# Optimization experiments

Hardware: AMD Instinct MI355X
Metric: run time of the kernel (lower is better)

Reference implementation:

```python
import jax, jax.numpy as jnp
import numpy as np

B, N, S = 32, 1000, 200
D, H, DK, FF, NL = 128, 8, 16, 512, 3
HK = H * DK


def _mha(x, Wq, Wk, Wv, Wo, bo):
    # x: [B, L, D]; manual multi-head attention matching the torch code
    Bv, L, _ = x.shape
    q = (x @ Wq).reshape(Bv, L, H, DK).transpose(0, 2, 1, 3)  # [B,H,L,dk]
    k = (x @ Wk).reshape(Bv, L, H, DK).transpose(0, 2, 1, 3)
    v = (x @ Wv).reshape(Bv, L, H, DK).transpose(0, 2, 1, 3)
    score = jnp.einsum('bhid,bhjd->bhij', q, k) / jnp.sqrt(jnp.asarray(DK, x.dtype))
    w = jax.nn.softmax(score, axis=-1)
    o = jnp.einsum('bhij,bhjd->bhid', w, v).transpose(0, 2, 1, 3).reshape(Bv, L, HK)
    return o @ Wo + bo


def _decoder_layer(x, Wq, Wk, Wv, Wo, bo, W1, b1, W2, b2):
    out1 = x + _mha(x, Wq, Wk, Wv, Wo, bo)
    ff = jax.nn.relu(out1 @ W1 + b1) @ W2 + b2
    return out1 + ff


def _forward(data, attention_bias, Wfirst, bfirst, Wlast, blast,
             Wq, Wk, Wv, Wo, bo, W1, b1, W2, b2, Wfin, bfin, sel):
    Bv, Np, Dm = data.shape
    Sn = sel.shape[1]
    bidx = jnp.arange(Bv)
    # _get_new_data: ordered list of unselected node indices, shape [B, N-S]
    mask = jnp.zeros((Bv, Np), bool).at[bidx[:, None], sel].set(True)
    vals = jnp.where(mask, Np, jnp.arange(Np)[None, :])
    unselect = jnp.sort(vals, axis=1)[:, : Np - Sn]            # [B, N-S]
    left = jnp.take_along_axis(data, unselect[:, :, None], axis=1)  # [B, N-S, D]
    # _get_encoding for first / last selected node
    first = data[bidx, sel[:, 0]]
    last = data[bidx, sel[:, -1]]
    ef = first @ Wfirst + bfirst
    el = last @ Wlast + blast
    out = jnp.concatenate([ef[:, None], left, el[:, None]], axis=1)  # [B, N-S+2, D]
    for i in range(Wq.shape[0]):
        out = _decoder_layer(out, Wq[i], Wk[i], Wv[i], Wo[i], bo[i],
                             W1[i], b1[i], W2[i], b2[i])
    logits = (out @ Wfin + bfin)[..., 0]                       # [B, N-S+2]
    # attention bias of current (last selected) node, gathered at unselected
    ab_cur = attention_bias[bidx, sel[:, -1]]                  # [B, N]
    ab_uns = jnp.take_along_axis(ab_cur, unselect, axis=1)     # [B, N-S]
    logits = logits.at[:, 1:-1].add(ab_uns)
    L = logits.shape[1]
    pos = jnp.arange(L)
    end_mask = (pos == 0) | (pos == L - 1)
    logits = jnp.where(end_mask[None, :], -jnp.inf, logits)
    props = jax.nn.softmax(logits, axis=-1)[:, 1:-1]           # [B, N-S]
    props = jnp.where(props <= 1e-5, props + 1e-7, props)
    # scatter back: selected positions -> -2, unselected -> props
    new_props = jnp.full((Bv, Np), -2.0, dtype=data.dtype)
    new_props = new_props.at[bidx[:, None], unselect].set(props)
    return new_props


def setup_inputs() -> dict:
    key = jax.random.key(0)
    ks = jax.random.split(key, 24)
    data = jax.random.normal(ks[0], (B, N, D), jnp.float32)
    # selected_node_list must contain unique indices per row (partial tour)
    sel = jax.vmap(lambda k: jax.random.permutation(k, N))(
        jax.random.split(ks[1], B))[:, :S].astype(jnp.int32)
    attention_bias = jax.random.normal(ks[2], (B, N, N), jnp.float32)

    def lin(k, shape, fan_in):
        return jax.random.normal(k, shape, jnp.float32) / np.float32(np.sqrt(fan_in))

    return dict(
        data=data,
        attention_bias=attention_bias,
        Wfirst=lin(ks[3], (D, D), D), bfirst=jnp.zeros((D,), jnp.float32),
        Wlast=lin(ks[4], (D, D), D), blast=jnp.zeros((D,), jnp.float32),
        Wq=lin(ks[5], (NL, D, HK), D),
        Wk=lin(ks[6], (NL, D, HK), D),
        Wv=lin(ks[7], (NL, D, HK), D),
        Wo=lin(ks[8], (NL, HK, D), HK), bo=jnp.zeros((NL, D), jnp.float32),
        W1=lin(ks[9], (NL, D, FF), D), b1=jnp.zeros((NL, FF), jnp.float32),
        W2=lin(ks[10], (NL, FF, D), FF), b2=jnp.zeros((NL, D), jnp.float32),
        Wfin=lin(ks[11], (D, 1), D), bfin=jnp.zeros((1,), jnp.float32),
        selected_node_list=sel,
    )


def reference(data, attention_bias, Wfirst, bfirst, Wlast, blast,
              Wq, Wk, Wv, Wo, bo, W1, b1, W2, b2, Wfin, bfin,
              selected_node_list):
    return _forward(data, attention_bias, Wfirst, bfirst, Wlast, blast,
                    Wq, Wk, Wv, Wo, bo, W1, b1, W2, b2, Wfin, bfin,
                    selected_node_list)
```

## Files before the change

### kernel.cpp

```cpp
#include <hip/hip_runtime.h>
#include <hip/hip_bf16.h>
#include <math.h>

#define NB 32
#define NN 1000
#define SS 200
#define DD 128
#define HH 8
#define DKK 16
#define FFD 512
#define NLAYER 3
#define LQ 802
#define LPAD 832
#define MROWS (NB*LQ)
#define NBLK64 (MROWS/64)
#define NQT 26
#define HSTR 516

typedef __attribute__((ext_vector_type(8))) short short8;
typedef __attribute__((ext_vector_type(4))) short short4v;
typedef __attribute__((ext_vector_type(16))) float f32x16;

static __device__ __forceinline__ unsigned short f2bf(float x) {
  union { float f; unsigned int u; } v; v.f = x;
  unsigned int r = v.u + 0x7fff + ((v.u >> 16) & 1);
  return (unsigned short)(r >> 16);
}

#define WCH 196608
__global__ __launch_bounds__(256) void k_wconv(const float* __restrict__ Wq, const float* __restrict__ Wk,
                       const float* __restrict__ Wv, const float* __restrict__ Wo,
                       const float* __restrict__ W1, const float* __restrict__ W2,
                       unsigned short* __restrict__ WtQKV, unsigned short* __restrict__ Wot,
                       unsigned short* __restrict__ W1t, unsigned short* __restrict__ W2t) {
  int e = blockIdx.x*256 + threadIdx.x;
  if (e >= 3*WCH) return;
  int layer = e / WCH, r = e - layer*WCH;
  if (r < 49152) {
    int n = r >> 7, k = r & 127;
    int sect = n >> 7, nn = n & 127;
    const float* W = (sect == 0) ? Wq : (sect == 1) ? Wk : Wv;
    WtQKV[layer*49152 + r] = f2bf(W[layer*16384 + k*128 + nn]);
  } else if (r < 65536) {
    int r2 = r - 49152;
    int n = r2 >> 7, k = r2 & 127;
    Wot[layer*16384 + r2] = f2bf(Wo[layer*16384 + k*128 + n]);
  } else if (r < 131072) {
    int r2 = r - 65536;
    int n = r2 >> 7, k = r2 & 127;
    W1t[layer*65536 + r2] = f2bf(W1[layer*65536 + k*512 + n]);
  } else {
    int r2 = r - 131072;
    int n = r2 >> 9, k = r2 & 511;
    W2t[layer*65536 + r2] = f2bf(W2[layer*65536 + k*128 + n]);
  }
}

__global__ __launch_bounds__(1024) void k_unselect(const int* __restrict__ sel,
                                                   int* __restrict__ unselect,
                                                   int* __restrict__ pos) {
  int b = blockIdx.x;
  int n = threadIdx.x;
  __shared__ int bufA[1024];
  __shared__ int bufB[1024];
  bufA[n] = (n < NN) ? 1 : 0;
  __syncthreads();
  if (n < SS) bufA[sel[b*SS + n]] = 0;
  __syncthreads();
  int flag = bufA[n];
  int* src = bufA; int* dst = bufB;
  for (int off = 1; off < 1024; off <<= 1) {
    int v = src[n];
    if (n >= off) v += src[n - off];
    __syncthreads();
    dst[n] = v;
    __syncthreads();
    int* tp = src; src = dst; dst = tp;
  }
  if (n < NN) {
    if (flag) {
      int j = src[n] - 1;
      unselect[b*800 + j] = n;
      pos[b*NN + n] = j + 1;
    } else {
      pos[b*NN + n] = -1;
    }
  }
}

__global__ __launch_bounds__(128) void k_embed(const float* __restrict__ data,
                       const int* __restrict__ sel, const int* __restrict__ unselect,
                       const float* __restrict__ Wfirst, const float* __restrict__ bfirst,
                       const float* __restrict__ Wlast, const float* __restrict__ blast,
                       float* __restrict__ X, unsigned short* __restrict__ Xbf) {
  int l = blockIdx.x, b = blockIdx.y, d = threadIdx.x;
  size_t off = ((size_t)(b*LQ + l))*DD + d;
  float val;
  if (l == 0 || l == LQ-1) {
    __shared__ float xr[DD];
    int src = sel[b*SS + (l == 0 ? 0 : SS-1)];
    const float* W    = (l == 0) ? Wfirst : Wlast;
    const float* bias = (l == 0) ? bfirst : blast;
    xr[d] = data[((size_t)b*NN + src)*DD + d];
    __syncthreads();
    float acc = bias[d];
    #pragma unroll 4
    for (int k = 0; k < DD; ++k) acc += xr[k] * W[k*DD + d];
    val = acc;
  } else {
    int nidx = unselect[b*800 + (l-1)];
    val = data[((size_t)b*NN + nidx)*DD + d];
  }
  X[off] = val;
  Xbf[off] = f2bf(val);
}

__global__ __launch_bounds__(256) void k_qkv_mfma(const unsigned short* __restrict__ Xbf,
                       const unsigned short* __restrict__ Wt,
                       unsigned short* __restrict__ Qb, unsigned short* __restrict__ Kb,
                       unsigned short* __restrict__ Vt) {
  int row0 = blockIdx.x * 64;
  int t = threadIdx.x, wave = t >> 6, lane = t & 63;
  int col = lane & 31, half = lane >> 5;
  short8 a[2][8];
  const unsigned short* xb = Xbf + (size_t)(row0 + col)*DD + half*8;
  #pragma unroll
  for (int mi = 0; mi < 2; ++mi)
    #pragma unroll
    for (int s = 0; s < 8; ++s)
      a[mi][s] = *(const short8*)(xb + (size_t)mi*32*DD + s*16);
  #pragma unroll
  for (int nn = 0; nn < 3; ++nn) {
    int ni = wave*3 + nn;
    short8 bfr[8];
    const unsigned short* wb = Wt + (size_t)(ni*32 + col)*DD + half*8;
    #pragma unroll
    for (int s = 0; s < 8; ++s) bfr[s] = *(const short8*)(wb + s*16);
    f32x16 acc0 = {0.f,0.f,0.f,0.f,0.f,0.f,0.f,0.f,0.f,0.f,0.f,0.f,0.f,0.f,0.f,0.f};
    f32x16 acc1 = {0.f,0.f,0.f,0.f,0.f,0.f,0.f,0.f,0.f,0.f,0.f,0.f,0.f,0.f,0.f,0.f};
    #pragma unroll
    for (int s = 0; s < 8; ++s) {
      acc0 = __builtin_amdgcn_mfma_f32_32x32x16_bf16(a[0][s], bfr[s], acc0, 0, 0, 0);
      acc1 = __builtin_amdgcn_mfma_f32_32x32x16_bf16(a[1][s], bfr[s], acc1, 0, 0, 0);
    }
    int n = ni*32 + col;
    int sect = n >> 7, nc = n & 127;
    int h = nc >> 4, d = nc & 15;
    #pragma unroll
    for (int mi = 0; mi < 2; ++mi) {
      const f32x16& acc = mi ? acc1 : acc0;
      #pragma unroll
      for (int r = 0; r < 16; ++r) {
        int m = row0 + mi*32 + (r&3) + 8*(r>>2) + 4*half;
        int b_ = m / LQ, l = m - b_*LQ;
        size_t bh = (size_t)(b_*HH + h);
        float v = acc[r];
        if (sect == 0)      Qb[(bh*LQ + l)*DKK + d] = f2bf(v * 0.25f);
        else if (sect == 1) Kb[(bh*LQ + l)*DKK + d] = f2bf(v);
        else                Vt[(bh*DKK + d)*LPAD + l] = f2bf(v);
      }
    }
  }
}

__global__ __launch_bounds__(256) void k_attn3(const unsigned short* __restrict__ Q,
                       const unsigned short* __restrict__ K,
                       const unsigned short* __restrict__ Vt,
                       unsigned short* __restrict__ Obf) {
  int bid = blockIdx.x;
  int g = bid & 7, i = bid >> 3;
  int bhg = i / NQT, qt = i - bhg*NQT;
  int bh = bhg*8 + g;
  int b = bh >> 3, h = bh & 7;
  int q0 = qt*32;
  size_t bhLQ = (size_t)bh * LQ;
  int t = threadIdx.x;
  int wave = t >> 6, lane = t & 63;
  int col = lane & 31;
  int half = lane >> 5;
  bool hb = (half != 0);

  __shared__ float mw[4][32];
  __shared__ float sw[4][32];
  __shared__ float sfin[32];
  __shared__ float ored[4][16][32];
  __shared__ float osum[32][17];

  int q = q0 + col; if (q > LQ-1) q = LQ-1;
  short8 bQ = *(const short8*)&Q[(bhLQ + q)*DKK + half*8];

  f32x16 oacc = {0.f,0.f,0.f,0.f,0.f,0.f,0.f,0.f,0.f,0.f,0.f,0.f,0.f,0.f,0.f,0.f};
  float runm = -INFINITY, runs = 0.f;

  for (int kt = wave; kt < NQT; kt += 4) {
    int key0 = kt*32;
    int keyA = key0 + col; if (keyA > LQ-1) keyA = LQ-1;
    short8 aK = *(const short8*)&K[(bhLQ + keyA)*DKK + half*8];
    f32x16 c = {0.f,0.f,0.f,0.f,0.f,0.f,0.f,0.f,0.f,0.f,0.f,0.f,0.f,0.f,0.f,0.f};
    c = __builtin_amdgcn_mfma_f32_32x32x16_bf16(aK, bQ, c, 0, 0, 0);
    bool full = (key0 + 31 < LQ);
    float tm;
    if (full) {
      tm = c[0];
      #pragma unroll
      for (int r = 1; r < 16; ++r) tm = fmaxf(tm, c[r]);
    } else {
      tm = -INFINITY;
      #pragma unroll
      for (int r = 0; r < 16; ++r) {
        int key = key0 + (r&3) + 8*(r>>2) + 4*half;
        if (key < LQ) tm = fmaxf(tm, c[r]);
      }
    }
    tm = fmaxf(tm, __shfl_xor(tm, 32, 64));
    float mnew = fmaxf(runm, tm);
    float scale = __expf(runm - mnew);
    runs *= scale;
    #pragma unroll
    for (int r = 0; r < 8; ++r) oacc[r] *= scale;
    runm = mnew;
    float p[16];
    if (full) {
      #pragma unroll
      for (int r = 0; r < 16; ++r) p[r] = __expf(c[r] - mnew);
    } else {
      #pragma unroll
      for (int r = 0; r < 16; ++r) {
        int key = key0 + (r&3) + 8*(r>>2) + 4*half;
        p[r] = (key < LQ) ? __expf(c[r] - mnew) : 0.f;
      }
    }
    float ts = 0.f;
    #pragma unroll
    for (int r = 0; r < 16; ++r) ts += p[r];
    runs += ts;
    unsigned int pk[8];
    #pragma unroll
    for (int j = 0; j < 8; ++j) {
      unsigned int ua = __float_as_uint(p[2*j]);
      unsigned int ub = __float_as_uint(p[2*j+1]);
      pk[j] = (ua >> 16) | (ub & 0xffff0000u);
    }
    int Y0 = __shfl_xor((int)(hb ? pk[0] : pk[2]), 32, 64);
    int Y1 = __shfl_xor((int)(hb ? pk[1] : pk[3]), 32, 64);
    int Y2 = __shfl_xor((int)(hb ? pk[4] : pk[6]), 32, 64);
    int Y3 = __shfl_xor((int)(hb ? pk[5] : pk[7]), 32, 64);
    union { int4 i4; short8 s8; } fA, fB;
    fA.i4.x = hb ? Y0 : (int)pk[0];
    fA.i4.y = hb ? Y1 : (int)pk[1];
    fA.i4.z = hb ? (int)pk[2] : Y0;
    fA.i4.w = hb ? (int)pk[3] : Y1;
    fB.i4.x = hb ? Y2 : (int)pk[4];
    fB.i4.y = hb ? Y3 : (int)pk[5];
    fB.i4.z = hb ? (int)pk[6] : Y2;
    fB.i4.w = hb ? (int)pk[7] : Y3;
    short8 aV0 = {0,0,0,0,0,0,0,0};
    short8 aV1 = {0,0,0,0,0,0,0,0};
    if (col < 16) {
      const unsigned short* vp = &Vt[((size_t)bh*DKK + col)*LPAD + key0 + half*8];
      aV0 = *(const short8*)vp;
      aV1 = *(const short8*)(vp + 16);
    }
    oacc = __builtin_amdgcn_mfma_f32_32x32x16_bf16(aV0, fA.s8, oacc, 0, 0, 0);
    oacc = __builtin_amdgcn_mfma_f32_32x32x16_bf16(aV1, fB.s8, oacc, 0, 0, 0);
  }

  float pm = __shfl_xor(runm, 32, 64);
  float ps = __shfl_xor(runs, 32, 64);
  float m2 = fmaxf(runm, pm);
  float fself = __expf(runm - m2);
  float s2 = runs*fself + ps*__expf(pm - m2);
  #pragma unroll
  for (int r = 0; r < 8; ++r) oacc[r] *= fself;
  if (half == 0) { mw[wave][col] = m2; sw[wave][col] = s2; }
  __syncthreads();
  float M = fmaxf(fmaxf(mw[0][col], mw[1][col]), fmaxf(mw[2][col], mw[3][col]));
  float S = sw[0][col]*__expf(mw[0][col]-M) + sw[1][col]*__expf(mw[1][col]-M)
          + sw[2][col]*__expf(mw[2][col]-M) + sw[3][col]*__expf(mw[3][col]-M);
  float fw = __expf(m2 - M);
  #pragma unroll
  for (int r = 0; r < 8; ++r) {
    int dv = (r&3) + 8*(r>>2) + 4*half;
    ored[wave][dv][col] = oacc[r] * fw;
  }
  if (wave == 0 && half == 0) sfin[col] = S;
  __syncthreads();
  {
    int qq = t & 31, dv0 = t >> 5;
    #pragma unroll
    for (int k = 0; k < 2; ++k) {
      int dv = dv0 + 8*k;
      osum[qq][dv] = ored[0][dv][qq] + ored[1][dv][qq] + ored[2][dv][qq] + ored[3][dv][qq];
    }
  }
  __syncthreads();
  {
    int qs = t >> 3, c2 = (t & 7)*2;
    if (q0 + qs < LQ) {
      float invS = 1.f / sfin[qs];
      unsigned int lo = f2bf(osum[qs][c2]   * invS);
      unsigned int hi = f2bf(osum[qs][c2+1] * invS);
      *(unsigned int*)&Obf[((size_t)(b*LQ + q0 + qs))*DD + h*DKK + c2] = lo | (hi << 16);
    }
  }
}

__global__ __launch_bounds__(256) void k_proj_mfma(const unsigned short* __restrict__ Obf,
                       const unsigned short* __restrict__ Wot,
                       const float* __restrict__ bo,
                       float* __restrict__ X, unsigned short* __restrict__ Xbf) {
  int row0 = blockIdx.x * 64;
  int t = threadIdx.x, wave = t >> 6, lane = t & 63;
  int col = lane & 31, half = lane >> 5;
  short8 a[2][8];
  const unsigned short* ob = Obf + (size_t)(row0 + col)*DD + half*8;
  #pragma unroll
  for (int mi = 0; mi < 2; ++mi)
    #pragma unroll
    for (int s = 0; s < 8; ++s)
      a[mi][s] = *(const short8*)(ob + (size_t)mi*32*DD + s*16);
  int ni = wave;
  short8 bfr[8];
  const unsigned short* wb = Wot + (size_t)(ni*32 + col)*DD + half*8;
  #pragma unroll
  for (int s = 0; s < 8; ++s) bfr[s] = *(const short8*)(wb + s*16);
  f32x16 acc0 = {0.f,0.f,0.f,0.f,0.f,0.f,0.f,0.f,0.f,0.f,0.f,0.f,0.f,0.f,0.f,0.f};
  f32x16 acc1 = {0.f,0.f,0.f,0.f,0.f,0.f,0.f,0.f,0.f,0.f,0.f,0.f,0.f,0.f,0.f,0.f};
  #pragma unroll
  for (int s = 0; s < 8; ++s) {
    acc0 = __builtin_amdgcn_mfma_f32_32x32x16_bf16(a[0][s], bfr[s], acc0, 0, 0, 0);
    acc1 = __builtin_amdgcn_mfma_f32_32x32x16_bf16(a[1][s], bfr[s], acc1, 0, 0, 0);
  }
  int n = ni*32 + col;
  float bv = bo[n];
  #pragma unroll
  for (int mi = 0; mi < 2; ++mi) {
    const f32x16& acc = mi ? acc1 : acc0;
    #pragma unroll
    for (int r = 0; r < 16; ++r) {
      int m = row0 + mi*32 + (r&3) + 8*(r>>2) + 4*half;
      size_t off = (size_t)m*DD + n;
      float res = X[off] + acc[r] + bv;
      X[off] = res;
      Xbf[off] = f2bf(res);
    }
  }
}

__global__ __launch_bounds__(256) void k_ff_mfma(const unsigned short* __restrict__ Xbf_in,
                       const unsigned short* __restrict__ W1t,
                       const float* __restrict__ b1,
                       const unsigned short* __restrict__ W2t,
                       const float* __restrict__ b2,
                       float* __restrict__ X, unsigned short* __restrict__ Xbf) {
  __shared__ __align__(16) unsigned short Hs[64 * HSTR];
  int row0 = blockIdx.x * 64;
  int t = threadIdx.x, wave = t >> 6, lane = t & 63;
  int col = lane & 31, half = lane >> 5;
  short8 a[2][8];
  const unsigned short* xb = Xbf_in + (size_t)(row0 + col)*DD + half*8;
  #pragma unroll
  for (int mi = 0; mi < 2; ++mi)
    #pragma unroll
    for (int s = 0; s < 8; ++s)
      a[mi][s] = *(const short8*)(xb + (size_t)mi*32*DD + s*16);
  #pragma unroll
  for (int nn = 0; nn < 4; ++nn) {
    int ni = wave*4 + nn;
    short8 bfr[8];
    const unsigned short* wb = W1t + (size_t)(ni*32 + col)*DD + half*8;
    #pragma unroll
    for (int s = 0; s < 8; ++s) bfr[s] = *(const short8*)(wb + s*16);
    f32x16 acc0 = {0.f,0.f,0.f,0.f,0.f,0.f,0.f,0.f,0.f,0.f,0.f,0.f,0.f,0.f,0.f,0.f};
    f32x16 acc1 = {0.f,0.f,0.f,0.f,0.f,0.f,0.f,0.f,0.f,0.f,0.f,0.f,0.f,0.f,0.f,0.f};
    #pragma unroll
    for (int s = 0; s < 8; ++s) {
      acc0 = __builtin_amdgcn_mfma_f32_32x32x16_bf16(a[0][s], bfr[s], acc0, 0, 0, 0);
      acc1 = __builtin_amdgcn_mfma_f32_32x32x16_bf16(a[1][s], bfr[s], acc1, 0, 0, 0);
    }
    int n = ni*32 + col;
    float bv = b1[n];
    #pragma unroll
    for (int mi = 0; mi < 2; ++mi) {
      const f32x16& acc = mi ? acc1 : acc0;
      #pragma unroll
      for (int r = 0; r < 16; ++r) {
        int ml = mi*32 + (r&3) + 8*(r>>2) + 4*half;
        Hs[ml*HSTR + n] = f2bf(fmaxf(acc[r] + bv, 0.f));
      }
    }
  }
  __syncthreads();
  int ni = wave;
  f32x16 acc0 = {0.f,0.f,0.f,0.f,0.f,0.f,0.f,0.f,0.f,0.f,0.f,0.f,0.f,0.f,0.f,0.f};
  f32x16 acc1 = {0.f,0.f,0.f,0.f,0.f,0.f,0.f,0.f,0.f,0.f,0.f,0.f,0.f,0.f,0.f,0.f};
  const unsigned short* w2b = W2t + (size_t)(ni*32 + col)*FFD + half*8;
  #pragma unroll 4
  for (int s = 0; s < 32; ++s) {
    int ko = s*16 + half*8;
    union { short4v h[2]; short8 v; } h0, h1;
    const unsigned short* hp0 = &Hs[col*HSTR + ko];
    const unsigned short* hp1 = &Hs[(32 + col)*HSTR + ko];
    h0.h[0] = *(const short4v*)hp0;  h0.h[1] = *(const short4v*)(hp0 + 4);
    h1.h[0] = *(const short4v*)hp1;  h1.h[1] = *(const short4v*)(hp1 + 4);
    short8 bfr = *(const short8*)(w2b + s*16);
    acc0 = __builtin_amdgcn_mfma_f32_32x32x16_bf16(h0.v, bfr, acc0, 0, 0, 0);
    acc1 = __builtin_amdgcn_mfma_f32_32x32x16_bf16(h1.v, bfr, acc1, 0, 0, 0);
  }
  int n = ni*32 + col;
  float bv = b2[n];
  #pragma unroll
  for (int mi = 0; mi < 2; ++mi) {
    const f32x16& acc = mi ? acc1 : acc0;
    #pragma unroll
    for (int r = 0; r < 16; ++r) {
      int m = row0 + mi*32 + (r&3) + 8*(r>>2) + 4*half;
      size_t off = (size_t)m*DD + n;
      float res = X[off] + acc[r] + bv;
      X[off] = res;
      Xbf[off] = f2bf(res);
    }
  }
}

__global__ __launch_bounds__(128) void k_logits(const float* __restrict__ X,
                        const float* __restrict__ Wfin, const float* __restrict__ bfin,
                        float* __restrict__ logits) {
  int row = blockIdx.x, t = threadIdx.x;
  float v = X[(size_t)row*DD + t] * Wfin[t];
  #pragma unroll
  for (int off = 32; off > 0; off >>= 1) v += __shfl_down(v, off);
  __shared__ float s2[2];
  if ((t & 63) == 0) s2[t >> 6] = v;
  __syncthreads();
  if (t == 0) logits[row] = s2[0] + s2[1] + bfin[0];
}

__global__ __launch_bounds__(256) void k_final(const float* __restrict__ logits,
                       const float* __restrict__ AB, const int* __restrict__ sel,
                       const int* __restrict__ unselect, const int* __restrict__ pos,
                       float* __restrict__ out) {
  int b = blockIdx.x, t = threadIdx.x;
  __shared__ float sl[800];
  __shared__ float red[256];
  int lastsel = sel[b*SS + SS-1];
  const float* abrow = AB + ((size_t)b*NN + lastsel)*NN;
  for (int j = t; j < 800; j += 256)
    sl[j] = logits[b*LQ + j + 1] + abrow[unselect[b*800 + j]];
  __syncthreads();
  float lm = -INFINITY;
  for (int j = t; j < 800; j += 256) lm = fmaxf(lm, sl[j]);
  red[t] = lm;
  __syncthreads();
  for (int s = 128; s > 0; s >>= 1) {
    if (t < s) red[t] = fmaxf(red[t], red[t+s]);
    __syncthreads();
  }
  float m = red[0];
  __syncthreads();
  float ls = 0.f;
  for (int j = t; j < 800; j += 256) ls += __expf(sl[j] - m);
  red[t] = ls;
  __syncthreads();
  for (int s = 128; s > 0; s >>= 1) {
    if (t < s) red[t] += red[t+s];
    __syncthreads();
  }
  float inv = 1.f / red[0];
  for (int n = t; n < NN; n += 256) {
    int p1 = pos[b*NN + n];
    float v = -2.0f;
    if (p1 >= 0) {
      float p = __expf(sl[p1-1] - m) * inv;
      if (p <= 1e-5f) p += 1e-7f;
      v = p;
    }
    out[(size_t)b*NN + n] = v;
  }
}

extern "C" void kernel_launch(void* const* d_in, const int* in_sizes, int n_in,
                              void* d_out, int out_size, void* d_ws, size_t ws_size,
                              hipStream_t stream) {
  const float* data   = (const float*)d_in[0];
  const float* AB     = (const float*)d_in[1];
  const float* Wfirst = (const float*)d_in[2];
  const float* bfirst = (const float*)d_in[3];
  const float* Wlast  = (const float*)d_in[4];
  const float* blast  = (const float*)d_in[5];
  const float* Wq     = (const float*)d_in[6];
  const float* Wk     = (const float*)d_in[7];
  const float* Wv     = (const float*)d_in[8];
  const float* Wo     = (const float*)d_in[9];
  const float* bo     = (const float*)d_in[10];
  const float* W1     = (const float*)d_in[11];
  const float* b1     = (const float*)d_in[12];
  const float* W2     = (const float*)d_in[13];
  const float* b2     = (const float*)d_in[14];
  const float* Wfin   = (const float*)d_in[15];
  const float* bfin   = (const float*)d_in[16];
  const int*   sel    = (const int*)d_in[17];
  float* out = (float*)d_out;
  (void)in_sizes; (void)n_in; (void)out_size; (void)ws_size;

  char* ws = (char*)d_ws;
  const size_t NELT = (size_t)MROWS * DD;
  int*   UNSEL = (int*)ws;
  int*   POS   = (int*)(ws + 102400);
  float* X     = (float*)(ws + 230400);
  unsigned short* Xbf = (unsigned short*)(X + NELT);
  unsigned short* Ob  = Xbf + NELT;
  unsigned short* Qb  = Ob + NELT;
  unsigned short* Kb  = Qb + (size_t)NB*HH*LQ*DKK;
  unsigned short* Vt  = Kb + (size_t)NB*HH*LQ*DKK;
  unsigned short* WtQKV = Vt + (size_t)NB*HH*DKK*LPAD;
  unsigned short* Wot = WtQKV + (size_t)NLAYER*384*128;
  unsigned short* W1t = Wot + (size_t)NLAYER*128*128;
  unsigned short* W2t = W1t + (size_t)NLAYER*512*128;
  float* LOG = (float*)(W2t + (size_t)NLAYER*128*512);

  k_wconv<<<(3*WCH + 255)/256, 256, 0, stream>>>(Wq, Wk, Wv, Wo, W1, W2, WtQKV, Wot, W1t, W2t);
  k_unselect<<<NB, 1024, 0, stream>>>(sel, UNSEL, POS);
  k_embed<<<dim3(LQ, NB), 128, 0, stream>>>(data, sel, UNSEL, Wfirst, bfirst, Wlast, blast, X, Xbf);
  for (int i = 0; i < NLAYER; ++i) {
    k_qkv_mfma<<<NBLK64, 256, 0, stream>>>(Xbf, WtQKV + (size_t)i*384*128, Qb, Kb, Vt);
    k_attn3<<<NQT*HH*NB, 256, 0, stream>>>(Qb, Kb, Vt, Ob);
    k_proj_mfma<<<NBLK64, 256, 0, stream>>>(Ob, Wot + (size_t)i*128*128, bo + (size_t)i*DD, X, Xbf);
    k_ff_mfma<<<NBLK64, 256, 0, stream>>>(Xbf, W1t + (size_t)i*512*128, b1 + (size_t)i*FFD,
                                          W2t + (size_t)i*128*512, b2 + (size_t)i*DD, X, Xbf);
  }
  k_logits<<<MROWS, 128, 0, stream>>>(X, Wfin, bfin, LOG);
  k_final<<<NB, 256, 0, stream>>>(LOG, AB, sel, UNSEL, POS, out);
}
```

Baseline: 580.3 us.

## Fuse out-projection with FFN, widen attention query tiles, vectorize embed and logits

Merges the output projection and feed-forward kernels into one kernel that keeps the post-attention residual in registers and its bf16 copy in LDS, so the X/Xbf round trip to global memory between them is avoided. The attention kernel now handles 64 queries per block, reusing each loaded K/V tile for two query sub-tiles. V is stored row-major instead of transposed and is gathered element by element. Embedding is split into a small kernel for the two end rows and a float4 gather for the middle rows, and the logits kernel computes four rows per block with one wave each. The scalar strided V gathers and the extra register and LDS pressure in attention could offset part of the gain.

```diff
diff --git a/kernel.cpp b/kernel.cpp
--- a/kernel.cpp
+++ b/kernel.cpp
@@ -11,11 +11,12 @@
 #define FFD 512
 #define NLAYER 3
 #define LQ 802
-#define LPAD 832
 #define MROWS (NB*LQ)
 #define NBLK64 (MROWS/64)
 #define NQT 26
+#define NQT64 13
 #define HSTR 516
+#define TSTR 132
 
 typedef __attribute__((ext_vector_type(8))) short short8;
 typedef __attribute__((ext_vector_type(4))) short short4v;
@@ -88,37 +89,47 @@
   }
 }
 
-__global__ __launch_bounds__(128) void k_embed(const float* __restrict__ data,
-                       const int* __restrict__ sel, const int* __restrict__ unselect,
+__global__ __launch_bounds__(128) void k_embed_ends(const float* __restrict__ data,
+                       const int* __restrict__ sel,
                        const float* __restrict__ Wfirst, const float* __restrict__ bfirst,
                        const float* __restrict__ Wlast, const float* __restrict__ blast,
                        float* __restrict__ X, unsigned short* __restrict__ Xbf) {
-  int l = blockIdx.x, b = blockIdx.y, d = threadIdx.x;
+  int which = blockIdx.x, b = blockIdx.y, d = threadIdx.x;
+  int l = (which == 0) ? 0 : LQ-1;
+  __shared__ float xr[DD];
+  int src = sel[b*SS + (which == 0 ? 0 : SS-1)];
+  const float* W    = (which == 0) ? Wfirst : Wlast;
+  const float* bias = (which == 0) ? bfirst : blast;
+  xr[d] = data[((size_t)b*NN + src)*DD + d];
+  __syncthreads();
+  float acc = bias[d];
+  #pragma unroll 4
+  for (int k = 0; k < DD; ++k) acc += xr[k] * W[k*DD + d];
   size_t off = ((size_t)(b*LQ + l))*DD + d;
-  float val;
-  if (l == 0 || l == LQ-1) {
-    __shared__ float xr[DD];
-    int src = sel[b*SS + (l == 0 ? 0 : SS-1)];
-    const float* W    = (l == 0) ? Wfirst : Wlast;
-    const float* bias = (l == 0) ? bfirst : blast;
-    xr[d] = data[((size_t)b*NN + src)*DD + d];
-    __syncthreads();
-    float acc = bias[d];
-    #pragma unroll 4
-    for (int k = 0; k < DD; ++k) acc += xr[k] * W[k*DD + d];
-    val = acc;
-  } else {
-    int nidx = unselect[b*800 + (l-1)];
-    val = data[((size_t)b*NN + nidx)*DD + d];
-  }
-  X[off] = val;
-  Xbf[off] = f2bf(val);
+  X[off] = acc;
+  Xbf[off] = f2bf(acc);
+}
+
+__global__ __launch_bounds__(256) void k_embed_mid(const float* __restrict__ data,
+                       const int* __restrict__ unselect,
+                       float* __restrict__ X, unsigned short* __restrict__ Xbf) {
+  int e = blockIdx.x*256 + threadIdx.x;
+  int r = e >> 5;
+  int c4 = (e & 31) * 4;
+  int b = r / 800, j = r - b*800;
+  int nidx = unselect[r];
+  const float4 v = *(const float4*)&data[((size_t)b*NN + nidx)*DD + c4];
+  size_t off = ((size_t)(b*LQ + 1 + j))*DD + c4;
+  *(float4*)&X[off] = v;
+  unsigned short p0 = f2bf(v.x), p1 = f2bf(v.y), p2 = f2bf(v.z), p3 = f2bf(v.w);
+  ushort4 pk; pk.x = p0; pk.y = p1; pk.z = p2; pk.w = p3;
+  *(ushort4*)&Xbf[off] = pk;
 }
 
 __global__ __launch_bounds__(256) void k_qkv_mfma(const unsigned short* __restrict__ Xbf,
                        const unsigned short* __restrict__ Wt,
                        unsigned short* __restrict__ Qb, unsigned short* __restrict__ Kb,
-                       unsigned short* __restrict__ Vt) {
+                       unsigned short* __restrict__ Vb) {
   int row0 = blockIdx.x * 64;
   int t = threadIdx.x, wave = t >> 6, lane = t & 63;
   int col = lane & 31, half = lane >> 5;
@@ -157,7 +168,7 @@
         float v = acc[r];
         if (sect == 0)      Qb[(bh*LQ + l)*DKK + d] = f2bf(v * 0.25f);
         else if (sect == 1) Kb[(bh*LQ + l)*DKK + d] = f2bf(v);
-        else                Vt[(bh*DKK + d)*LPAD + l] = f2bf(v);
+        else                Vb[(bh*LQ + l)*DKK + d] = f2bf(v);
       }
     }
   }
@@ -165,14 +176,14 @@
 
 __global__ __launch_bounds__(256) void k_attn3(const unsigned short* __restrict__ Q,
                        const unsigned short* __restrict__ K,
-                       const unsigned short* __restrict__ Vt,
+                       const unsigned short* __restrict__ Vb,
                        unsigned short* __restrict__ Obf) {
   int bid = blockIdx.x;
   int g = bid & 7, i = bid >> 3;
-  int bhg = i / NQT, qt = i - bhg*NQT;
+  int bhg = i / NQT64, qt = i - bhg*NQT64;
   int bh = bhg*8 + g;
   int b = bh >> 3, h = bh & 7;
-  int q0 = qt*32;
+  int q0 = qt*64;
   size_t bhLQ = (size_t)bh * LQ;
   int t = threadIdx.x;
   int wave = t >> 6, lane = t & 63;
@@ -180,190 +191,219 @@
   int half = lane >> 5;
   bool hb = (half != 0);
 
-  __shared__ float mw[4][32];
-  __shared__ float sw[4][32];
-  __shared__ float sfin[32];
-  __shared__ float ored[4][16][32];
-  __shared__ float osum[32][17];
-
-  int q = q0 + col; if (q > LQ-1) q = LQ-1;
-  short8 bQ = *(const short8*)&Q[(bhLQ + q)*DKK + half*8];
-
-  f32x16 oacc = {0.f,0.f,0.f,0.f,0.f,0.f,0.f,0.f,0.f,0.f,0.f,0.f,0.f,0.f,0.f,0.f};
-  float runm = -INFINITY, runs = 0.f;
+  __shared__ float mw[2][4][32];
+  __shared__ float sw[2][4][32];
+  __shared__ float sfin[2][32];
+  __shared__ float ored[2][4][16][32];
+  __shared__ float osum[2][32][17];
+
+  int q0c = q0 + col;      if (q0c > LQ-1) q0c = LQ-1;
+  int q1c = q0 + 32 + col; if (q1c > LQ-1) q1c = LQ-1;
+  short8 bQ0 = *(const short8*)&Q[(bhLQ + q0c)*DKK + half*8];
+  short8 bQ1 = *(const short8*)&Q[(bhLQ + q1c)*DKK + half*8];
+
+  f32x16 oacc0 = {0.f,0.f,0.f,0.f,0.f,0.f,0.f,0.f,0.f,0.f,0.f,0.f,0.f,0.f,0.f,0.f};
+  f32x16 oacc1 = oacc0;
+  float runm0 = -INFINITY, runs0 = 0.f;
+  float runm1 = -INFINITY, runs1 = 0.f;
 
   for (int kt = wave; kt < NQT; kt += 4) {
     int key0 = kt*32;
     int keyA = key0 + col; if (keyA > LQ-1) keyA = LQ-1;
     short8 aK = *(const short8*)&K[(bhLQ + keyA)*DKK + half*8];
-    f32x16 c = {0.f,0.f,0.f,0.f,0.f,0.f,0.f,0.f,0.f,0.f,0.f,0.f,0.f,0.f,0.f,0.f};
-    c = __builtin_amdgcn_mfma_f32_32x32x16_bf16(aK, bQ, c, 0, 0, 0);
-    bool full = (key0 + 31 < LQ);
-    float tm;
-    if (full) {
-      tm = c[0];
-      #pragma unroll
-      for (int r = 1; r < 16; ++r) tm = fmaxf(tm, c[r]);
-    } else {
-      tm = -INFINITY;
-      #pragma unroll
-      for (int r = 0; r < 16; ++r) {
-        int key = key0 + (r&3) + 8*(r>>2) + 4*half;
-        if (key < LQ) tm = fmaxf(tm, c[r]);
-      }
-    }
-    tm = fmaxf(tm, __shfl_xor(tm, 32, 64));
-    float mnew = fmaxf(runm, tm);
-    float scale = __expf(runm - mnew);
-    runs *= scale;
-    #pragma unroll
-    for (int r = 0; r < 8; ++r) oacc[r] *= scale;
-    runm = mnew;
-    float p[16];
-    if (full) {
-      #pragma unroll
-      for (int r = 0; r < 16; ++r) p[r] = __expf(c[r] - mnew);
-    } else {
-      #pragma unroll
-      for (int r = 0; r < 16; ++r) {
-        int key = key0 + (r&3) + 8*(r>>2) + 4*half;
-        p[r] = (key < LQ) ? __expf(c[r] - mnew) : 0.f;
-      }
-    }
-    float ts = 0.f;
-    #pragma unroll
-    for (int r = 0; r < 16; ++r) ts += p[r];
-    runs += ts;
-    unsigned int pk[8];
-    #pragma unroll
-    for (int j = 0; j < 8; ++j) {
-      unsigned int ua = __float_as_uint(p[2*j]);
-      unsigned int ub = __float_as_uint(p[2*j+1]);
-      pk[j] = (ua >> 16) | (ub & 0xffff0000u);
-    }
-    int Y0 = __shfl_xor((int)(hb ? pk[0] : pk[2]), 32, 64);
-    int Y1 = __shfl_xor((int)(hb ? pk[1] : pk[3]), 32, 64);
-    int Y2 = __shfl_xor((int)(hb ? pk[4] : pk[6]), 32, 64);
-    int Y3 = __shfl_xor((int)(hb ? pk[5] : pk[7]), 32, 64);
-    union { int4 i4; short8 s8; } fA, fB;
-    fA.i4.x = hb ? Y0 : (int)pk[0];
-    fA.i4.y = hb ? Y1 : (int)pk[1];
-    fA.i4.z = hb ? (int)pk[2] : Y0;
-    fA.i4.w = hb ? (int)pk[3] : Y1;
-    fB.i4.x = hb ? Y2 : (int)pk[4];
-    fB.i4.y = hb ? Y3 : (int)pk[5];
-    fB.i4.z = hb ? (int)pk[6] : Y2;
-    fB.i4.w = hb ? (int)pk[7] : Y3;
     short8 aV0 = {0,0,0,0,0,0,0,0};
     short8 aV1 = {0,0,0,0,0,0,0,0};
     if (col < 16) {
-      const unsigned short* vp = &Vt[((size_t)bh*DKK + col)*LPAD + key0 + half*8];
-      aV0 = *(const short8*)vp;
-      aV1 = *(const short8*)(vp + 16);
-    }
-    oacc = __builtin_amdgcn_mfma_f32_32x32x16_bf16(aV0, fA.s8, oacc, 0, 0, 0);
-    oacc = __builtin_amdgcn_mfma_f32_32x32x16_bf16(aV1, fB.s8, oacc, 0, 0, 0);
-  }
-
-  float pm = __shfl_xor(runm, 32, 64);
-  float ps = __shfl_xor(runs, 32, 64);
-  float m2 = fmaxf(runm, pm);
-  float fself = __expf(runm - m2);
-  float s2 = runs*fself + ps*__expf(pm - m2);
-  #pragma unroll
-  for (int r = 0; r < 8; ++r) oacc[r] *= fself;
-  if (half == 0) { mw[wave][col] = m2; sw[wave][col] = s2; }
-  __syncthreads();
-  float M = fmaxf(fmaxf(mw[0][col], mw[1][col]), fmaxf(mw[2][col], mw[3][col]));
-  float S = sw[0][col]*__expf(mw[0][col]-M) + sw[1][col]*__expf(mw[1][col]-M)
-          + sw[2][col]*__expf(mw[2][col]-M) + sw[3][col]*__expf(mw[3][col]-M);
-  float fw = __expf(m2 - M);
-  #pragma unroll
-  for (int r = 0; r < 8; ++r) {
-    int dv = (r&3) + 8*(r>>2) + 4*half;
-    ored[wave][dv][col] = oacc[r] * fw;
-  }
-  if (wave == 0 && half == 0) sfin[col] = S;
+      const unsigned short* vbase = Vb + bhLQ*DKK + col;
+      #pragma unroll
+      for (int j = 0; j < 8; ++j) {
+        int k1 = key0 + half*8 + j;      if (k1 > LQ-1) k1 = LQ-1;
+        int k2 = key0 + 16 + half*8 + j; if (k2 > LQ-1) k2 = LQ-1;
+        aV0[j] = (short)vbase[(size_t)k1*DKK];
+        aV1[j] = (short)vbase[(size_t)k2*DKK];
+      }
+    }
+    bool full = (key0 + 31 < LQ);
+
+    auto process = [&](const short8& bQ, f32x16& oacc, float& runm, float& runs) {
+      f32x16 c = {0.f,0.f,0.f,0.f,0.f,0.f,0.f,0.f,0.f,0.f,0.f,0.f,0.f,0.f,0.f,0.f};
+      c = __builtin_amdgcn_mfma_f32_32x32x16_bf16(aK, bQ, c, 0, 0, 0);
+      float tm;
+      if (full) {
+        tm = c[0];
+        #pragma unroll
+        for (int r = 1; r < 16; ++r) tm = fmaxf(tm, c[r]);
+      } else {
+        tm = -INFINITY;
+        #pragma unroll
+        for (int r = 0; r < 16; ++r) {
+          int key = key0 + (r&3) + 8*(r>>2) + 4*half;
+          if (key < LQ) tm = fmaxf(tm, c[r]);
+        }
+      }
+      tm = fmaxf(tm, __shfl_xor(tm, 32, 64));
+      float mnew = fmaxf(runm, tm);
+      float scale = __expf(runm - mnew);
+      runs *= scale;
+      #pragma unroll
+      for (int r = 0; r < 8; ++r) oacc[r] *= scale;
+      runm = mnew;
+      float p[16];
+      if (full) {
+        #pragma unroll
+        for (int r = 0; r < 16; ++r) p[r] = __expf(c[r] - mnew);
+      } else {
+        #pragma unroll
+        for (int r = 0; r < 16; ++r) {
+          int key = key0 + (r&3) + 8*(r>>2) + 4*half;
+          p[r] = (key < LQ) ? __expf(c[r] - mnew) : 0.f;
+        }
+      }
+      float ts = 0.f;
+      #pragma unroll
+      for (int r = 0; r < 16; ++r) ts += p[r];
+      runs += ts;
+      unsigned int pk[8];
+      #pragma unroll
+      for (int j = 0; j < 8; ++j) {
+        unsigned int ua = __float_as_uint(p[2*j]);
+        unsigned int ub = __float_as_uint(p[2*j+1]);
+        pk[j] = (ua >> 16) | (ub & 0xffff0000u);
+      }
+      int Y0 = __shfl_xor((int)(hb ? pk[0] : pk[2]), 32, 64);
+      int Y1 = __shfl_xor((int)(hb ? pk[1] : pk[3]), 32, 64);
+      int Y2 = __shfl_xor((int)(hb ? pk[4] : pk[6]), 32, 64);
+      int Y3 = __shfl_xor((int)(hb ? pk[5] : pk[7]), 32, 64);
+      union { int4 i4; short8 s8; } fA, fB;
+      fA.i4.x = hb ? Y0 : (int)pk[0];
+      fA.i4.y = hb ? Y1 : (int)pk[1];
+      fA.i4.z = hb ? (int)pk[2] : Y0;
+      fA.i4.w = hb ? (int)pk[3] : Y1;
+      fB.i4.x = hb ? Y2 : (int)pk[4];
+      fB.i4.y = hb ? Y3 : (int)pk[5];
+      fB.i4.z = hb ? (int)pk[6] : Y2;
+      fB.i4.w = hb ? (int)pk[7] : Y3;
+      oacc = __builtin_amdgcn_mfma_f32_32x32x16_bf16(aV0, fA.s8, oacc, 0, 0, 0);
+      oacc = __builtin_amdgcn_mfma_f32_32x32x16_bf16(aV1, fB.s8, oacc, 0, 0, 0);
+    };
+    process(bQ0, oacc0, runm0, runs0);
+    process(bQ1, oacc1, runm1, runs1);
+  }
+
+  float m2v[2], fsv[2];
+  #pragma unroll
+  for (int u = 0; u < 2; ++u) {
+    float runm = u ? runm1 : runm0;
+    float runs = u ? runs1 : runs0;
+    float pm = __shfl_xor(runm, 32, 64);
+    float ps = __shfl_xor(runs, 32, 64);
+    float m2 = fmaxf(runm, pm);
+    float fself = __expf(runm - m2);
+    float s2 = runs*fself + ps*__expf(pm - m2);
+    if (half == 0) { mw[u][wave][col] = m2; sw[u][wave][col] = s2; }
+    m2v[u] = m2; fsv[u] = fself;
+  }
+  __syncthreads();
+  #pragma unroll
+  for (int u = 0; u < 2; ++u) {
+    float M = fmaxf(fmaxf(mw[u][0][col], mw[u][1][col]), fmaxf(mw[u][2][col], mw[u][3][col]));
+    float S = sw[u][0][col]*__expf(mw[u][0][col]-M) + sw[u][1][col]*__expf(mw[u][1][col]-M)
+            + sw[u][2][col]*__expf(mw[u][2][col]-M) + sw[u][3][col]*__expf(mw[u][3][col]-M);
+    float fw = __expf(m2v[u] - M) * fsv[u];
+    const f32x16& oacc = u ? oacc1 : oacc0;
+    #pragma unroll
+    for (int r = 0; r < 8; ++r) {
+      int dv = (r&3) + 8*(r>>2) + 4*half;
+      ored[u][wave][dv][col] = oacc[r] * fw;
+    }
+    if (wave == 0 && half == 0) sfin[u][col] = S;
+  }
   __syncthreads();
   {
     int qq = t & 31, dv0 = t >> 5;
     #pragma unroll
-    for (int k = 0; k < 2; ++k) {
-      int dv = dv0 + 8*k;
-      osum[qq][dv] = ored[0][dv][qq] + ored[1][dv][qq] + ored[2][dv][qq] + ored[3][dv][qq];
-    }
+    for (int u = 0; u < 2; ++u)
+      #pragma unroll
+      for (int k = 0; k < 2; ++k) {
+        int dv = dv0 + 8*k;
+        osum[u][qq][dv] = ored[u][0][dv][qq] + ored[u][1][dv][qq]
+                        + ored[u][2][dv][qq] + ored[u][3][dv][qq];
+      }
   }
   __syncthreads();
   {
     int qs = t >> 3, c2 = (t & 7)*2;
-    if (q0 + qs < LQ) {
-      float invS = 1.f / sfin[qs];
-      unsigned int lo = f2bf(osum[qs][c2]   * invS);
-      unsigned int hi = f2bf(osum[qs][c2+1] * invS);
-      *(unsigned int*)&Obf[((size_t)(b*LQ + q0 + qs))*DD + h*DKK + c2] = lo | (hi << 16);
-    }
-  }
-}
-
-__global__ __launch_bounds__(256) void k_proj_mfma(const unsigned short* __restrict__ Obf,
-                       const unsigned short* __restrict__ Wot,
-                       const float* __restrict__ bo,
-                       float* __restrict__ X, unsigned short* __restrict__ Xbf) {
+    #pragma unroll
+    for (int u = 0; u < 2; ++u) {
+      int q = q0 + u*32 + qs;
+      if (q < LQ) {
+        float invS = 1.f / sfin[u][qs];
+        unsigned int lo = f2bf(osum[u][qs][c2]   * invS);
+        unsigned int hi = f2bf(osum[u][qs][c2+1] * invS);
+        *(unsigned int*)&Obf[((size_t)(b*LQ + q))*DD + h*DKK + c2] = lo | (hi << 16);
+      }
+    }
+  }
+}
+
+__global__ __launch_bounds__(256) void k_pff(const unsigned short* __restrict__ Obf,
+        const unsigned short* __restrict__ Wot, const float* __restrict__ bo,
+        const unsigned short* __restrict__ W1t, const float* __restrict__ b1,
+        const unsigned short* __restrict__ W2t, const float* __restrict__ b2,
+        float* __restrict__ X, unsigned short* __restrict__ Xbf) {
+  __shared__ __align__(16) unsigned short LDSU[64 * HSTR];
+  unsigned short* T  = LDSU;
+  unsigned short* Hs = LDSU;
   int row0 = blockIdx.x * 64;
   int t = threadIdx.x, wave = t >> 6, lane = t & 63;
   int col = lane & 31, half = lane >> 5;
-  short8 a[2][8];
-  const unsigned short* ob = Obf + (size_t)(row0 + col)*DD + half*8;
+  int n = wave*32 + col;
+  float res[2][16];
+  {
+    short8 a[2][8];
+    const unsigned short* ob = Obf + (size_t)(row0 + col)*DD + half*8;
+    #pragma unroll
+    for (int mi = 0; mi < 2; ++mi)
+      #pragma unroll
+      for (int s = 0; s < 8; ++s)
+        a[mi][s] = *(const short8*)(ob + (size_t)mi*32*DD + s*16);
+    short8 bfr[8];
+    const unsigned short* wb = Wot + (size_t)n*DD + half*8;
+    #pragma unroll
+    for (int s = 0; s < 8; ++s) bfr[s] = *(const short8*)(wb + s*16);
+    f32x16 acc0 = {0.f,0.f,0.f,0.f,0.f,0.f,0.f,0.f,0.f,0.f,0.f,0.f,0.f,0.f,0.f,0.f};
+    f32x16 acc1 = acc0;
+    #pragma unroll
+    for (int s = 0; s < 8; ++s) {
+      acc0 = __builtin_amdgcn_mfma_f32_32x32x16_bf16(a[0][s], bfr[s], acc0, 0, 0, 0);
+      acc1 = __builtin_amdgcn_mfma_f32_32x32x16_bf16(a[1][s], bfr[s], acc1, 0, 0, 0);
+    }
+    float bv = bo[n];
+    #pragma unroll
+    for (int mi = 0; mi < 2; ++mi) {
+      const f32x16& acc = mi ? acc1 : acc0;
+      #pragma unroll
+      for (int r = 0; r < 16; ++r) {
+        int ml = mi*32 + (r&3) + 8*(r>>2) + 4*half;
+        size_t off = (size_t)(row0 + ml)*DD + n;
+        res[mi][r] = X[off] + acc[r] + bv;
+        T[ml*TSTR + n] = f2bf(res[mi][r]);
+      }
+    }
+  }
+  __syncthreads();
+  short8 aF[2][8];
   #pragma unroll
   for (int mi = 0; mi < 2; ++mi)
     #pragma unroll
-    for (int s = 0; s < 8; ++s)
-      a[mi][s] = *(const short8*)(ob + (size_t)mi*32*DD + s*16);
-  int ni = wave;
-  short8 bfr[8];
-  const unsigned short* wb = Wot + (size_t)(ni*32 + col)*DD + half*8;
-  #pragma unroll
-  for (int s = 0; s < 8; ++s) bfr[s] = *(const short8*)(wb + s*16);
-  f32x16 acc0 = {0.f,0.f,0.f,0.f,0.f,0.f,0.f,0.f,0.f,0.f,0.f,0.f,0.f,0.f,0.f,0.f};
-  f32x16 acc1 = {0.f,0.f,0.f,0.f,0.f,0.f,0.f,0.f,0.f,0.f,0.f,0.f,0.f,0.f,0.f,0.f};
-  #pragma unroll
-  for (int s = 0; s < 8; ++s) {
-    acc0 = __builtin_amdgcn_mfma_f32_32x32x16_bf16(a[0][s], bfr[s], acc0, 0, 0, 0);
-    acc1 = __builtin_amdgcn_mfma_f32_32x32x16_bf16(a[1][s], bfr[s], acc1, 0, 0, 0);
-  }
-  int n = ni*32 + col;
-  float bv = bo[n];
-  #pragma unroll
-  for (int mi = 0; mi < 2; ++mi) {
-    const f32x16& acc = mi ? acc1 : acc0;
-    #pragma unroll
-    for (int r = 0; r < 16; ++r) {
-      int m = row0 + mi*32 + (r&3) + 8*(r>>2) + 4*half;
-      size_t off = (size_t)m*DD + n;
-      float res = X[off] + acc[r] + bv;
-      X[off] = res;
-      Xbf[off] = f2bf(res);
-    }
-  }
-}
-
-__global__ __launch_bounds__(256) void k_ff_mfma(const unsigned short* __restrict__ Xbf_in,
-                       const unsigned short* __restrict__ W1t,
-                       const float* __restrict__ b1,
-                       const unsigned short* __restrict__ W2t,
-                       const float* __restrict__ b2,
-                       float* __restrict__ X, unsigned short* __restrict__ Xbf) {
-  __shared__ __align__(16) unsigned short Hs[64 * HSTR];
-  int row0 = blockIdx.x * 64;
-  int t = threadIdx.x, wave = t >> 6, lane = t & 63;
-  int col = lane & 31, half = lane >> 5;
-  short8 a[2][8];
-  const unsigned short* xb = Xbf_in + (size_t)(row0 + col)*DD + half*8;
-  #pragma unroll
-  for (int mi = 0; mi < 2; ++mi)
-    #pragma unroll
-    for (int s = 0; s < 8; ++s)
-      a[mi][s] = *(const short8*)(xb + (size_t)mi*32*DD + s*16);
+    for (int s = 0; s < 8; ++s) {
+      const unsigned short* tp = &T[(mi*32 + col)*TSTR + half*8 + s*16];
+      union { short4v h[2]; short8 v; } u;
+      u.h[0] = *(const short4v*)tp;
+      u.h[1] = *(const short4v*)(tp + 4);
+      aF[mi][s] = u.v;
+    }
+  __syncthreads();
   #pragma unroll
   for (int nn = 0; nn < 4; ++nn) {
     int ni = wave*4 + nn;
@@ -372,29 +412,28 @@
     #pragma unroll
     for (int s = 0; s < 8; ++s) bfr[s] = *(const short8*)(wb + s*16);
     f32x16 acc0 = {0.f,0.f,0.f,0.f,0.f,0.f,0.f,0.f,0.f,0.f,0.f,0.f,0.f,0.f,0.f,0.f};
-    f32x16 acc1 = {0.f,0.f,0.f,0.f,0.f,0.f,0.f,0.f,0.f,0.f,0.f,0.f,0.f,0.f,0.f,0.f};
+    f32x16 acc1 = acc0;
     #pragma unroll
     for (int s = 0; s < 8; ++s) {
-      acc0 = __builtin_amdgcn_mfma_f32_32x32x16_bf16(a[0][s], bfr[s], acc0, 0, 0, 0);
-      acc1 = __builtin_amdgcn_mfma_f32_32x32x16_bf16(a[1][s], bfr[s], acc1, 0, 0, 0);
-    }
-    int n = ni*32 + col;
-    float bv = b1[n];
+      acc0 = __builtin_amdgcn_mfma_f32_32x32x16_bf16(aF[0][s], bfr[s], acc0, 0, 0, 0);
+      acc1 = __builtin_amdgcn_mfma_f32_32x32x16_bf16(aF[1][s], bfr[s], acc1, 0, 0, 0);
+    }
+    int nf = ni*32 + col;
+    float bv = b1[nf];
     #pragma unroll
     for (int mi = 0; mi < 2; ++mi) {
       const f32x16& acc = mi ? acc1 : acc0;
       #pragma unroll
       for (int r = 0; r < 16; ++r) {
         int ml = mi*32 + (r&3) + 8*(r>>2) + 4*half;
-        Hs[ml*HSTR + n] = f2bf(fmaxf(acc[r] + bv, 0.f));
-      }
-    }
-  }
-  __syncthreads();
-  int ni = wave;
+        Hs[ml*HSTR + nf] = f2bf(fmaxf(acc[r] + bv, 0.f));
+      }
+    }
+  }
+  __syncthreads();
   f32x16 acc0 = {0.f,0.f,0.f,0.f,0.f,0.f,0.f,0.f,0.f,0.f,0.f,0.f,0.f,0.f,0.f,0.f};
-  f32x16 acc1 = {0.f,0.f,0.f,0.f,0.f,0.f,0.f,0.f,0.f,0.f,0.f,0.f,0.f,0.f,0.f,0.f};
-  const unsigned short* w2b = W2t + (size_t)(ni*32 + col)*FFD + half*8;
+  f32x16 acc1 = acc0;
+  const unsigned short* w2b = W2t + (size_t)n*FFD + half*8;
   #pragma unroll 4
   for (int s = 0; s < 32; ++s) {
     int ko = s*16 + half*8;
@@ -407,33 +446,32 @@
     acc0 = __builtin_amdgcn_mfma_f32_32x32x16_bf16(h0.v, bfr, acc0, 0, 0, 0);
     acc1 = __builtin_amdgcn_mfma_f32_32x32x16_bf16(h1.v, bfr, acc1, 0, 0, 0);
   }
-  int n = ni*32 + col;
   float bv = b2[n];
   #pragma unroll
   for (int mi = 0; mi < 2; ++mi) {
     const f32x16& acc = mi ? acc1 : acc0;
     #pragma unroll
     for (int r = 0; r < 16; ++r) {
-      int m = row0 + mi*32 + (r&3) + 8*(r>>2) + 4*half;
-      size_t off = (size_t)m*DD + n;
-      float res = X[off] + acc[r] + bv;
-      X[off] = res;
-      Xbf[off] = f2bf(res);
-    }
-  }
-}
-
-__global__ __launch_bounds__(128) void k_logits(const float* __restrict__ X,
+      int ml = mi*32 + (r&3) + 8*(r>>2) + 4*half;
+      size_t off = (size_t)(row0 + ml)*DD + n;
+      float v = res[mi][r] + acc[r] + bv;
+      X[off] = v;
+      Xbf[off] = f2bf(v);
+    }
+  }
+}
+
+__global__ __launch_bounds__(256) void k_logits(const float* __restrict__ X,
                         const float* __restrict__ Wfin, const float* __restrict__ bfin,
                         float* __restrict__ logits) {
-  int row = blockIdx.x, t = threadIdx.x;
-  float v = X[(size_t)row*DD + t] * Wfin[t];
+  int t = threadIdx.x, wave = t >> 6, lane = t & 63;
+  int row = blockIdx.x*4 + wave;
+  float2 xv = *(const float2*)&X[(size_t)row*DD + lane*2];
+  float2 wv = *(const float2*)&Wfin[lane*2];
+  float v = xv.x*wv.x + xv.y*wv.y;
   #pragma unroll
   for (int off = 32; off > 0; off >>= 1) v += __shfl_down(v, off);
-  __shared__ float s2[2];
-  if ((t & 63) == 0) s2[t >> 6] = v;
-  __syncthreads();
-  if (t == 0) logits[row] = s2[0] + s2[1] + bfin[0];
+  if (lane == 0) logits[row] = v + bfin[0];
 }
 
 __global__ __launch_bounds__(256) void k_final(const float* __restrict__ logits,
@@ -512,8 +550,8 @@
   unsigned short* Ob  = Xbf + NELT;
   unsigned short* Qb  = Ob + NELT;
   unsigned short* Kb  = Qb + (size_t)NB*HH*LQ*DKK;
-  unsigned short* Vt  = Kb + (size_t)NB*HH*LQ*DKK;
-  unsigned short* WtQKV = Vt + (size_t)NB*HH*DKK*LPAD;
+  unsigned short* Vb  = Kb + (size_t)NB*HH*LQ*DKK;
+  unsigned short* WtQKV = Vb + (size_t)NB*HH*LQ*DKK;
   unsigned short* Wot = WtQKV + (size_t)NLAYER*384*128;
   unsigned short* W1t = Wot + (size_t)NLAYER*128*128;
   unsigned short* W2t = W1t + (size_t)NLAYER*512*128;
@@ -521,14 +559,15 @@
 
   k_wconv<<<(3*WCH + 255)/256, 256, 0, stream>>>(Wq, Wk, Wv, Wo, W1, W2, WtQKV, Wot, W1t, W2t);
   k_unselect<<<NB, 1024, 0, stream>>>(sel, UNSEL, POS);
-  k_embed<<<dim3(LQ, NB), 128, 0, stream>>>(data, sel, UNSEL, Wfirst, bfirst, Wlast, blast, X, Xbf);
+  k_embed_ends<<<dim3(2, NB), 128, 0, stream>>>(data, sel, Wfirst, bfirst, Wlast, blast, X, Xbf);
+  k_embed_mid<<<3200, 256, 0, stream>>>(data, UNSEL, X, Xbf);
   for (int i = 0; i < NLAYER; ++i) {
-    k_qkv_mfma<<<NBLK64, 256, 0, stream>>>(Xbf, WtQKV + (size_t)i*384*128, Qb, Kb, Vt);
-    k_attn3<<<NQT*HH*NB, 256, 0, stream>>>(Qb, Kb, Vt, Ob);
-    k_proj_mfma<<<NBLK64, 256, 0, stream>>>(Ob, Wot + (size_t)i*128*128, bo + (size_t)i*DD, X, Xbf);
-    k_ff_mfma<<<NBLK64, 256, 0, stream>>>(Xbf, W1t + (size_t)i*512*128, b1 + (size_t)i*FFD,
-                                          W2t + (size_t)i*128*512, b2 + (size_t)i*DD, X, Xbf);
-  }
-  k_logits<<<MROWS, 128, 0, stream>>>(X, Wfin, bfin, LOG);
+    k_qkv_mfma<<<NBLK64, 256, 0, stream>>>(Xbf, WtQKV + (size_t)i*384*128, Qb, Kb, Vb);
+    k_attn3<<<NQT64*HH*NB, 256, 0, stream>>>(Qb, Kb, Vb, Ob);
+    k_pff<<<NBLK64, 256, 0, stream>>>(Ob, Wot + (size_t)i*128*128, bo + (size_t)i*DD,
+                                      W1t + (size_t)i*512*128, b1 + (size_t)i*FFD,
+                                      W2t + (size_t)i*128*512, b2 + (size_t)i*DD, X, Xbf);
+  }
+  k_logits<<<MROWS/4, 256, 0, stream>>>(X, Wfin, bfin, LOG);
   k_final<<<NB, 256, 0, stream>>>(LOG, AB, sel, UNSEL, POS, out);
 }
```

Result: no change. 572.7 us (-1.3%).
